# Kernel optimization log

Measured on AMD Instinct MI355X. Metric: run time of the kernel, lower is better.

The kernel has to match this reference:

```python
import jax, jax.numpy as jnp
import numpy as np

B, N, NODE_DIM = 256, 200, 2
H, D, L, FF = 8, 128, 3, 512
KD = D // H  # key/val dim per head = 16
EPS = 1e-5


def _uniform(key, shape, fan):
    s = 1.0 / np.sqrt(fan)
    return jax.random.uniform(key, shape, jnp.float32, -s, s)


def setup_inputs() -> dict:
    key = jax.random.key(0)
    ks = jax.random.split(key, 16)
    return {
        "x": jax.random.normal(ks[0], (B, N, NODE_DIM), jnp.float32),
        "Wemb": _uniform(ks[1], (NODE_DIM, D), NODE_DIM),
        "bemb": _uniform(ks[2], (D,), NODE_DIM),
        "Wq": _uniform(ks[3], (L, H, D, KD), KD),
        "Wk": _uniform(ks[4], (L, H, D, KD), KD),
        "Wv": _uniform(ks[5], (L, H, D, KD), KD),
        "Wo": _uniform(ks[6], (L, H, KD, D), D),
        "bn1_g": jnp.ones((L, D), jnp.float32),
        "bn1_b": jnp.zeros((L, D), jnp.float32),
        "W1": _uniform(ks[7], (L, D, FF), D),
        "b1": _uniform(ks[8], (L, FF), D),
        "W2": _uniform(ks[9], (L, FF, D), FF),
        "b2": _uniform(ks[10], (L, D), FF),
        "bn2_g": jnp.ones((L, D), jnp.float32),
        "bn2_b": jnp.zeros((L, D), jnp.float32),
    }


def _batch_norm(h, g, b):
    # BatchNorm1d in training mode: stats over all (batch*graph) positions per channel
    hf = h.reshape(-1, h.shape[-1])
    m = hf.mean(axis=0)
    v = hf.var(axis=0)  # biased variance, as torch uses for normalization
    return (h - m) * jax.lax.rsqrt(v + EPS) * g + b


def _mha(h, Wq, Wk, Wv, Wo):
    # h: [B,N,D]; Wq/Wk/Wv: [H,D,KD]; Wo: [H,KD,D]
    Q = jnp.einsum('bnd,hdk->hbnk', h, Wq)
    K = jnp.einsum('bnd,hdk->hbnk', h, Wk)
    V = jnp.einsum('bnd,hdk->hbnk', h, Wv)
    scores = jnp.einsum('hbqk,hbnk->hbqn', Q, K) * (1.0 / np.sqrt(KD))
    attn = jax.nn.softmax(scores, axis=-1)
    heads = jnp.einsum('hbqn,hbnk->hbqk', attn, V)
    return jnp.einsum('hbqk,hkd->bqd', heads, Wo)


def reference(x, Wemb, bemb, Wq, Wk, Wv, Wo, bn1_g, bn1_b, W1, b1, W2, b2, bn2_g, bn2_b):
    h = x @ Wemb + bemb  # init_embed: [B,N,D]
    for l in range(L):
        h = h + _mha(h, Wq[l], Wk[l], Wv[l], Wo[l])
        h = _batch_norm(h, bn1_g[l], bn1_b[l])
        ff = jax.nn.relu(h @ W1[l] + b1[l]) @ W2[l] + b2[l]
        h = _batch_norm(h + ff, bn2_g[l], bn2_b[l])
    return (h, h.mean(axis=1))
```

## Files before the change

kernel.cpp:

```cpp
#include <hip/hip_runtime.h>
#include <math.h>

#define B_ 256
#define N_ 200
#define D_ 128
#define H_ 8
#define KD_ 16
#define L_ 3
#define FF_ 512
#define ROWS (B_*N_)
#define BND (ROWS*D_)

typedef float f32x4 __attribute__((ext_vector_type(4)));
typedef _Float16 f16x4 __attribute__((ext_vector_type(4)));
typedef _Float16 f16x8 __attribute__((ext_vector_type(8)));

__device__ __forceinline__ ushort f2h_bits(float f) {
  _Float16 h = (_Float16)f;
  union { _Float16 h; ushort u; } v; v.h = h; return v.u;
}
__device__ __forceinline__ float h2f(ushort u) {
  union { ushort u; _Float16 h; } v; v.u = u; return (float)v.h;
}
__device__ __forceinline__ void bn_reduce(const float* psum, const float* psq,
    const float* gamma, const float* beta, int c, float& sc, float& sh) {
  if (gamma == nullptr) { sc = 1.f; sh = 0.f; return; }
  float s = psum[c], q = psq[c];
  const float invM = 1.f / 51200.f;
  float m = s * invM;
  float v = fmaf(q, invM, -m * m);
  float rr = rsqrtf(v + 1e-5f);
  sc = rr * gamma[c];
  sh = fmaf(-m, sc, beta[c]);
}

__global__ __launch_bounds__(256) void init_kernel(const float* __restrict__ x,
    const float* __restrict__ Wemb, const float* __restrict__ bemb,
    const float* __restrict__ Wo, const float* __restrict__ W2,
    ushort* __restrict__ h, ushort* __restrict__ woT, ushort* __restrict__ w2T,
    float* __restrict__ pa_s, float* __restrict__ pa_q,
    float* __restrict__ pb_s, float* __restrict__ pb_q)
{
  int blk = blockIdx.x, t = threadIdx.x;
  if (blk < 6400) {
    int i4 = blk * 256 + t;
    int r  = i4 >> 5, c4 = i4 & 31;
    float x0 = x[2*r], x1 = x[2*r + 1];
    const float4 w0 = ((const float4*)Wemb)[c4];
    const float4 w1 = ((const float4*)Wemb)[32 + c4];
    const float4 bb = ((const float4*)bemb)[c4];
    ushort o16[4];
    o16[0] = f2h_bits(fmaf(x0, w0.x, fmaf(x1, w1.x, bb.x)));
    o16[1] = f2h_bits(fmaf(x0, w0.y, fmaf(x1, w1.y, bb.y)));
    o16[2] = f2h_bits(fmaf(x0, w0.z, fmaf(x1, w1.z, bb.z)));
    o16[3] = f2h_bits(fmaf(x0, w0.w, fmaf(x1, w1.w, bb.w)));
    uint2 p;
    p.x = (uint)o16[0] | ((uint)o16[1] << 16);
    p.y = (uint)o16[2] | ((uint)o16[3] << 16);
    ((uint2*)h)[i4] = p;
  } else if (blk < 7360) {
    int i = (blk - 6400) * 256 + t;
    if (i < 49152) {
      int l = i / 16384, r = i % 16384;
      int n = r >> 7, k = r & 127;
      int hh = k >> 4, kd = k & 15;
      woT[i] = f2h_bits(Wo[l*16384 + hh*2048 + kd*128 + n]);
    } else {
      int j = i - 49152;
      int l = j / 65536, r = j % 65536;
      int d = r >> 9, f = r & 511;
      w2T[j] = f2h_bits(W2[l*65536 + f*128 + d]);
    }
  } else {
    if (t < 128) { pa_s[t] = 0.f; pa_q[t] = 0.f; pb_s[t] = 0.f; pb_q[t] = 0.f; }
  }
}

__global__ __launch_bounds__(128) void fold_qkv(const float* __restrict__ Wq,
    const float* __restrict__ Wk, const float* __restrict__ Wv,
    const float* __restrict__ pb_s, const float* __restrict__ pb_q,
    const float* __restrict__ gamma, const float* __restrict__ beta,
    ushort* __restrict__ wh, float* __restrict__ bout,
    float* __restrict__ scout, float* __restrict__ shout,
    float* __restrict__ pa_s, float* __restrict__ pa_q)
{
  __shared__ float wsum[2];
  int n = blockIdx.x;
  int k = threadIdx.x;
  float sc, sh;
  bn_reduce(pb_s, pb_q, gamma, beta, k, sc, sh);
  if (n == 0) { scout[k] = sc; shout[k] = sh; }
  if (n == 1) { pa_s[k] = 0.f; pa_q[k] = 0.f; }
  int which = n >> 7, hh = (n >> 4) & 7, kd = n & 15;
  const float* src = (which == 0) ? Wq : (which == 1) ? Wk : Wv;
  float w = src[hh*2048 + k*16 + kd];
  if (which == 0) w *= 0.25f * 1.44269504088896340736f;
  wh[n*128 + k] = f2h_bits(w * sc);
  float p = sh * w;
#pragma unroll
  for (int d = 1; d < 64; d <<= 1) p += __shfl_xor(p, d);
  if ((k & 63) == 0) wsum[k >> 6] = p;
  __syncthreads();
  if (k == 0) bout[n] = wsum[0] + wsum[1];
}

__global__ __launch_bounds__(128) void fold_w1(const float* __restrict__ W1,
    const float* __restrict__ b1,
    const float* __restrict__ pa_s, const float* __restrict__ pa_q,
    const float* __restrict__ gamma, const float* __restrict__ beta,
    ushort* __restrict__ wh, float* __restrict__ bout,
    float* __restrict__ scout, float* __restrict__ shout)
{
  __shared__ float wsum[2];
  int f = blockIdx.x;
  int k = threadIdx.x;
  float sc, sh;
  bn_reduce(pa_s, pa_q, gamma, beta, k, sc, sh);
  if (f == 0) { scout[k] = sc; shout[k] = sh; }
  float w = W1[k*512 + f];
  wh[f*128 + k] = f2h_bits(w * sc);
  float p = sh * w;
#pragma unroll
  for (int d = 1; d < 64; d <<= 1) p += __shfl_xor(p, d);
  if ((k & 63) == 0) wsum[k >> 6] = p;
  __syncthreads();
  if (k == 0) bout[f] = b1[f] + wsum[0] + wsum[1];
}

template<int K, bool BIAS, bool RELU, bool RESIDBN,
         bool OUTQKV, bool OUT16, bool STATS>
__global__ __launch_bounds__(256, 2) void gemm_mfma(
    const ushort* __restrict__ Ah,
    const ushort* __restrict__ Wh,
    const float* __restrict__ bias,
    const ushort* rh,
    const float* __restrict__ rsc, const float* __restrict__ rsh,
    ushort* o0, ushort* o1, ushort* o2,
    float* __restrict__ psum, float* __restrict__ psq, int Ntot)
{
  __shared__ ushort AhS[128*64];
  __shared__ ushort BhS[128*64];
  const int t    = threadIdx.x;
  const int nx   = gridDim.x;
  const int nwg  = nx * gridDim.y;
  const int lin  = blockIdx.y * nx + blockIdx.x;
  const int q8   = nwg >> 3, r8 = nwg & 7;
  const int xcd  = lin & 7, i8 = lin >> 3;
  const int wg   = (xcd < r8 ? xcd*(q8+1) : r8*(q8+1) + (xcd-r8)*q8) + i8;
  const int bm   = (wg / nx) * 128;
  const int bn   = (wg % nx) * 128;
  const int lane = t & 63;
  const int w    = t >> 6, wm = w >> 1, wn = w & 1;
  const int quad = lane >> 4, l15 = lane & 15;

  f32x4 acc[4][4];
#pragma unroll
  for (int i = 0; i < 4; i++)
#pragma unroll
    for (int j = 0; j < 4; j++) acc[i][j] = (f32x4){0.f, 0.f, 0.f, 0.f};

  const ushort* AhB = Ah + (size_t)bm * K;
  const ushort* BhB = Wh + (size_t)bn * K;

  for (int k0 = 0; k0 < K; k0 += 64) {
#pragma unroll
    for (int i = 0; i < 4; i++) {
      int idx = i * 256 + t;
      int row = idx >> 3, c = idx & 7;
      int k8  = c ^ (row & 7);
      size_t off = (size_t)row * K + k0 + k8 * 8;
      ((uint4*)AhS)[idx] = *(const uint4*)(AhB + off);
      ((uint4*)BhS)[idx] = *(const uint4*)(BhB + off);
    }
    __syncthreads();
#pragma unroll
    for (int ks = 0; ks < 2; ks++) {
      f16x8 ah[4], bh[4];
#pragma unroll
      for (int i = 0; i < 4; i++) {
        int row = wm * 64 + i * 16 + l15;
        int k8  = ks * 4 + quad;
        int ci  = k8 ^ (row & 7);
        ah[i] = ((const f16x8*)AhS)[row * 8 + ci];
        int nrow = wn * 64 + i * 16 + l15;
        int cj   = k8 ^ (nrow & 7);
        bh[i] = ((const f16x8*)BhS)[nrow * 8 + cj];
      }
#pragma unroll
      for (int i = 0; i < 4; i++)
#pragma unroll
        for (int j = 0; j < 4; j++)
          acc[i][j] = __builtin_amdgcn_mfma_f32_16x16x32_f16(ah[i], bh[j], acc[i][j], 0, 0, 0);
    }
    __syncthreads();
  }

  float bv[4], scv[4], shv[4];
#pragma unroll
  for (int j = 0; j < 4; j++) {
    int col = bn + wn*64 + j*16 + l15;
    if (BIAS)    bv[j]  = bias[col];
    if (RESIDBN) { scv[j] = rsc[col]; shv[j] = rsh[col]; }
  }
  float sj[4] = {0.f,0.f,0.f,0.f}, qj[4] = {0.f,0.f,0.f,0.f};
#pragma unroll
  for (int i = 0; i < 4; i++) {
#pragma unroll
    for (int r = 0; r < 4; r++) {
      int row = bm + wm*64 + i*16 + quad*4 + r;
#pragma unroll
      for (int j = 0; j < 4; j++) {
        int col = bn + wn*64 + j*16 + l15;
        float v = acc[i][j][r];
        if (BIAS)    v += bv[j];
        if (RELU)    v = fmaxf(v, 0.f);
        if (RESIDBN) {
          float rr = h2f(rh[(size_t)row * Ntot + col]);
          v += fmaf(rr, scv[j], shv[j]);
        }
        if (OUTQKV) {
          if (bn == 0) {
            o0[((size_t)(col >> 4) * ROWS + row) * 16 + (col & 15)] = f2h_bits(v);
          } else if (bn == 128) {
            int c = col - 128;
            o1[((size_t)(c >> 4) * ROWS + row) * 16 + (c & 15)] = f2h_bits(v);
          } else {
            int c = col - 256;
            o2[((size_t)(c >> 4) * ROWS + row) * 16 + (c & 15)] = f2h_bits(v);
          }
        }
        if (OUT16) o0[(size_t)row * Ntot + col] = f2h_bits(v);
        if (STATS) { sj[j] += v; qj[j] = fmaf(v, v, qj[j]); }
      }
    }
  }
  if (STATS) {
#pragma unroll
    for (int j = 0; j < 4; j++) {
      sj[j] += __shfl_xor(sj[j], 16); sj[j] += __shfl_xor(sj[j], 32);
      qj[j] += __shfl_xor(qj[j], 16); qj[j] += __shfl_xor(qj[j], 32);
    }
    float* ssum = (float*)AhS;
    float* ssq  = ssum + 128;
    if (t < 128) { ssum[t] = 0.f; ssq[t] = 0.f; }
    __syncthreads();
    if (quad == 0) {
#pragma unroll
      for (int j = 0; j < 4; j++) {
        int col = wn*64 + j*16 + l15;
        atomicAdd(&ssum[col], sj[j]);
        atomicAdd(&ssq[col],  qj[j]);
      }
    }
    __syncthreads();
    if (t < 128) {
      atomicAdd(&psum[t], ssum[t]);
      atomicAdd(&psq[t],  ssq[t]);
    }
  }
}

__global__ __launch_bounds__(256, 1) void ffn_fused(
    const ushort* __restrict__ h,
    const ushort* __restrict__ w1,
    const float* __restrict__ b1f,
    const ushort* __restrict__ w2t,
    const float* __restrict__ b2,
    const float* __restrict__ rsc, const float* __restrict__ rsh,
    ushort* hout,
    float* __restrict__ psum, float* __restrict__ psq)
{
  __shared__ ushort Ash[2*128*64];
  __shared__ ushort WB [2*128*64];
  __shared__ ushort HB [2*128*72];
  const int t    = threadIdx.x;
  const int bm   = blockIdx.x * 128;
  const int lane = t & 63;
  const int w    = t >> 6, wm = w >> 1, wn = w & 1;
  const int quad = lane >> 4, l15 = lane & 15;

  {
    const ushort* AB = h + (size_t)bm * 128;
    for (int half = 0; half < 2; half++)
#pragma unroll
      for (int i = 0; i < 4; i++) {
        int idx = i * 256 + t;
        int row = idx >> 3, c = idx & 7;
        int k8  = c ^ (row & 7);
        ((uint4*)(Ash + half*8192))[idx] = *(const uint4*)(AB + (size_t)row*128 + half*64 + k8*8);
      }
  }

  f32x4 aco[4][4];
#pragma unroll
  for (int i = 0; i < 4; i++)
#pragma unroll
    for (int j = 0; j < 4; j++) aco[i][j] = (f32x4){0.f, 0.f, 0.f, 0.f};

  __syncthreads();

  for (int ch = 0; ch < 4; ch++) {
    {
      const ushort* W1B = w1 + (size_t)ch * 128 * 128;
      for (int half = 0; half < 2; half++)
#pragma unroll
        for (int i = 0; i < 4; i++) {
          int idx = i * 256 + t;
          int row = idx >> 3, c = idx & 7;
          int k8  = c ^ (row & 7);
          ((uint4*)(WB + half*8192))[idx] = *(const uint4*)(W1B + (size_t)row*128 + half*64 + k8*8);
        }
    }
    __syncthreads();
    f32x4 ach[4][4];
#pragma unroll
    for (int i = 0; i < 4; i++)
#pragma unroll
      for (int j = 0; j < 4; j++) ach[i][j] = (f32x4){0.f, 0.f, 0.f, 0.f};
#pragma unroll
    for (int ks = 0; ks < 4; ks++) {
      int half = ks >> 1, k8 = (ks & 1)*4 + quad;
      f16x8 ah[4], bh[4];
#pragma unroll
      for (int i = 0; i < 4; i++) {
        int row = wm*64 + i*16 + l15;
        int ci  = k8 ^ (row & 7);
        ah[i] = ((const f16x8*)(Ash + half*8192))[row*8 + ci];
        int fr = wn*64 + i*16 + l15;
        int cj  = k8 ^ (fr & 7);
        bh[i] = ((const f16x8*)(WB + half*8192))[fr*8 + cj];
      }
#pragma unroll
      for (int i = 0; i < 4; i++)
#pragma unroll
        for (int j = 0; j < 4; j++)
          ach[i][j] = __builtin_amdgcn_mfma_f32_16x16x32_f16(ah[i], bh[j], ach[i][j], 0, 0, 0);
    }
    __syncthreads();
    {
      float bv1[4];
#pragma unroll
      for (int j = 0; j < 4; j++) bv1[j] = b1f[ch*128 + wn*64 + j*16 + l15];
#pragma unroll
      for (int i = 0; i < 4; i++)
#pragma unroll
        for (int r = 0; r < 4; r++) {
          int row = wm*64 + i*16 + quad*4 + r;
#pragma unroll
          for (int j = 0; j < 4; j++) {
            float hv = fmaxf(ach[i][j][r] + bv1[j], 0.f);
            int k6  = j*16 + l15;
            int ci8 = (k6 >> 3) ^ (row & 7);
            HB[(wn*128 + row)*72 + ci8*8 + (l15 & 7)] = f2h_bits(hv);
          }
        }
    }
    {
      const ushort* W2B = w2t + ch * 128;
      for (int half = 0; half < 2; half++)
#pragma unroll
        for (int i = 0; i < 4; i++) {
          int idx = i * 256 + t;
          int row = idx >> 3, c = idx & 7;
          int k8  = c ^ (row & 7);
          ((uint4*)(WB + half*8192))[idx] = *(const uint4*)(W2B + (size_t)row*512 + half*64 + k8*8);
        }
    }
    __syncthreads();
#pragma unroll
    for (int ks = 0; ks < 4; ks++) {
      int half = ks >> 1, k8 = (ks & 1)*4 + quad;
      f16x8 ah[4], bh[4];
#pragma unroll
      for (int i = 0; i < 4; i++) {
        int row = wm*64 + i*16 + l15;
        int ci  = k8 ^ (row & 7);
        ah[i] = *(const f16x8*)&HB[(half*128 + row)*72 + ci*8];
        int dr = wn*64 + i*16 + l15;
        int cj  = k8 ^ (dr & 7);
        bh[i] = ((const f16x8*)(WB + half*8192))[dr*8 + cj];
      }
#pragma unroll
      for (int i = 0; i < 4; i++)
#pragma unroll
        for (int j = 0; j < 4; j++)
          aco[i][j] = __builtin_amdgcn_mfma_f32_16x16x32_f16(ah[i], bh[j], aco[i][j], 0, 0, 0);
    }
    __syncthreads();
  }

  float bv[4], scv[4], shv[4];
#pragma unroll
  for (int j = 0; j < 4; j++) {
    int col = wn*64 + j*16 + l15;
    bv[j]  = b2[col];
    scv[j] = rsc[col]; shv[j] = rsh[col];
  }
  float sj[4] = {0.f,0.f,0.f,0.f}, qj[4] = {0.f,0.f,0.f,0.f};
#pragma unroll
  for (int i = 0; i < 4; i++) {
#pragma unroll
    for (int r = 0; r < 4; r++) {
      int rloc = wm*64 + i*16 + quad*4 + r;
      int row  = bm + rloc;
#pragma unroll
      for (int j = 0; j < 4; j++) {
        int col = wn*64 + j*16 + l15;
        float v = aco[i][j][r] + bv[j];
        int k6 = col & 63, half = col >> 6;
        int ci = (k6 >> 3) ^ (rloc & 7);
        float rr = h2f(Ash[half*8192 + rloc*64 + ci*8 + (k6 & 7)]);
        v += fmaf(rr, scv[j], shv[j]);
        hout[(size_t)row * 128 + col] = f2h_bits(v);
        sj[j] += v; qj[j] = fmaf(v, v, qj[j]);
      }
    }
  }
#pragma unroll
  for (int j = 0; j < 4; j++) {
    sj[j] += __shfl_xor(sj[j], 16); sj[j] += __shfl_xor(sj[j], 32);
    qj[j] += __shfl_xor(qj[j], 16); qj[j] += __shfl_xor(qj[j], 32);
  }
  __syncthreads();
  float* ssum = (float*)Ash;
  float* ssq  = ssum + 128;
  if (t < 128) { ssum[t] = 0.f; ssq[t] = 0.f; }
  __syncthreads();
  if (quad == 0) {
#pragma unroll
    for (int j = 0; j < 4; j++) {
      int col = wn*64 + j*16 + l15;
      atomicAdd(&ssum[col], sj[j]);
      atomicAdd(&ssq[col],  qj[j]);
    }
  }
  __syncthreads();
  if (t < 128) {
    atomicAdd(&psum[t], ssum[t]);
    atomicAdd(&psq[t],  ssq[t]);
  }
}

__global__ __launch_bounds__(256) void attn_kernel(const ushort* __restrict__ qs,
    const ushort* __restrict__ ks, const ushort* __restrict__ vh,
    ushort* __restrict__ hd, float* __restrict__ pb_s, float* __restrict__ pb_q)
{
  __shared__ __align__(16) _Float16 Ksh[208*24];
  __shared__ __align__(16) _Float16 VTh[16*216];
  const int b  = blockIdx.x >> 3;
  const int hh = blockIdx.x & 7;
  const int t  = threadIdx.x;
  if (blockIdx.x == 0 && t < 128) { pb_s[t] = 0.f; pb_q[t] = 0.f; }
  const size_t rb = (size_t)b * N_;
  const size_t hb = ((size_t)hh * ROWS + rb) * 16;

  for (int i = t; i < 208*2; i += 256) {
    int n = i >> 1, half = i & 1;
    uint4 kv = {0u, 0u, 0u, 0u};
    if (n < N_) kv = *(const uint4*)(ks + hb + n*16 + half*8);
    *(uint4*)&Ksh[n*24 + half*8] = kv;
  }
  for (int i = t; i < 208*2; i += 256) {
    int n = i >> 1, half = i & 1;
    uint4 v0 = {0u, 0u, 0u, 0u};
    if (n < N_) v0 = *(const uint4*)(vh + hb + n*16 + half*8);
    const ushort* e0 = (const ushort*)&v0;
#pragma unroll
    for (int q = 0; q < 8; q++)
      ((ushort*)VTh)[(half*8 + q)*216 + n] = e0[q];
  }
  __syncthreads();

  const int lane = t & 63;
  const int w    = t >> 6;
  const int l15  = lane & 15;
  const int g    = lane >> 4;

  for (int qt = w; qt < 13; qt += 4) {
    int qr  = qt*16 + l15;
    int qrc = qr < N_ ? qr : N_-1;
    f16x4 bq = *(const f16x4*)(qs + hb + (size_t)qrc*16 + g*4);

    f32x4 ct[13];
#pragma unroll
    for (int kt = 0; kt < 13; kt++) {
      f16x4 ak = *(const f16x4*)&Ksh[(kt*16 + l15)*24 + g*4];
      ct[kt] = __builtin_amdgcn_mfma_f32_16x16x16f16(ak, bq, (f32x4){0.f,0.f,0.f,0.f}, 0, 0, 0);
    }
#pragma unroll
    for (int r = 0; r < 4; r++)
      if (g*4 + r >= 8) ct[12][r] = -1e30f;

    float m0 = -1e30f, m1 = -1e30f;
#pragma unroll
    for (int kt = 0; kt < 13; kt++) {
      m0 = fmaxf(m0, fmaxf(ct[kt][0], ct[kt][1]));
      m1 = fmaxf(m1, fmaxf(ct[kt][2], ct[kt][3]));
    }
    float m = fmaxf(m0, m1);
    m = fmaxf(m, __shfl_xor(m, 16));
    m = fmaxf(m, __shfl_xor(m, 32));

    float la0 = 0.f, la1 = 0.f, la2 = 0.f, la3 = 0.f;
#pragma unroll
    for (int kt = 0; kt < 13; kt++) {
      float p0 = __builtin_amdgcn_exp2f(ct[kt][0] - m);
      float p1 = __builtin_amdgcn_exp2f(ct[kt][1] - m);
      float p2 = __builtin_amdgcn_exp2f(ct[kt][2] - m);
      float p3 = __builtin_amdgcn_exp2f(ct[kt][3] - m);
      la0 += p0; la1 += p1; la2 += p2; la3 += p3;
      ct[kt][0] = p0; ct[kt][1] = p1; ct[kt][2] = p2; ct[kt][3] = p3;
    }
    float l = (la0 + la1) + (la2 + la3);
    l += __shfl_xor(l, 16);
    l += __shfl_xor(l, 32);

    f32x4 och = {0.f,0.f,0.f,0.f};
#pragma unroll
    for (int kt = 0; kt < 13; kt++) {
      f16x4 pt = { (_Float16)ct[kt][0], (_Float16)ct[kt][1],
                   (_Float16)ct[kt][2], (_Float16)ct[kt][3] };
      f16x4 avh = *(const f16x4*)&VTh[l15*216 + kt*16 + g*4];
      och = __builtin_amdgcn_mfma_f32_16x16x16f16(avh, pt, och, 0, 0, 0);
    }

    if (qr < N_) {
      float inv = __builtin_amdgcn_rcpf(l);
      ushort o16[4];
#pragma unroll
      for (int r = 0; r < 4; r++) o16[r] = f2h_bits(och[r] * inv);
      uint2 p;
      p.x = (uint)o16[0] | ((uint)o16[1] << 16);
      p.y = (uint)o16[2] | ((uint)o16[3] << 16);
      *(uint2*)(hd + (rb + qr)*128 + hh*16 + g*4) = p;
    }
  }
}

__global__ __launch_bounds__(256) void bn_mean_final(const ushort* __restrict__ h,
    const float* __restrict__ pb_s, const float* __restrict__ pb_q,
    const float* __restrict__ gamma, const float* __restrict__ beta,
    float* __restrict__ outh, float* __restrict__ mout)
{
  __shared__ float part[2][128];
  int b = blockIdx.x;
  int t = threadIdx.x;
  int d = t & 127, half = t >> 7;
  float sc, sh;
  bn_reduce(pb_s, pb_q, gamma, beta, d, sc, sh);
  float s = 0.f;
  for (int n = half*100; n < half*100 + 100; n++) {
    size_t idx = ((size_t)b * N_ + n) * 128 + d;
    float v = fmaf(h2f(h[idx]), sc, sh);
    outh[idx] = v;
    s += v;
  }
  part[half][d] = s;
  __syncthreads();
  if (half == 0) mout[b * 128 + d] = (part[0][d] + part[1][d]) * (1.f / N_);
}

extern "C" void kernel_launch(void* const* d_in, const int* in_sizes, int n_in,
                              void* d_out, int out_size, void* d_ws, size_t ws_size,
                              hipStream_t stream)
{
  const float* x    = (const float*)d_in[0];
  const float* Wemb = (const float*)d_in[1];
  const float* bemb = (const float*)d_in[2];
  const float* Wq   = (const float*)d_in[3];
  const float* Wk   = (const float*)d_in[4];
  const float* Wv   = (const float*)d_in[5];
  const float* Wo   = (const float*)d_in[6];
  const float* bn1g = (const float*)d_in[7];
  const float* bn1b = (const float*)d_in[8];
  const float* W1   = (const float*)d_in[9];
  const float* b1   = (const float*)d_in[10];
  const float* W2   = (const float*)d_in[11];
  const float* b2   = (const float*)d_in[12];
  const float* bn2g = (const float*)d_in[13];
  const float* bn2b = (const float*)d_in[14];
  float* out = (float*)d_out;

  char* wsb = (char*)d_ws;
  ushort* h     = (ushort*)wsb;
  char*   phase = wsb + 13107200;
  ushort* qsb   = (ushort*)phase;
  ushort* ksb   = (ushort*)(phase + 13107200);
  ushort* vhh   = (ushort*)(phase + 26214400);
  ushort* hd    = (ushort*)(phase + 39321600);
  char*   wp    = wsb + 65536000;
  ushort* woT   = (ushort*)wp;
  ushort* w2T   = (ushort*)(wp + 98304);
  ushort* fqkvw = (ushort*)(wp + 491520);
  ushort* fw1w  = (ushort*)(wp + 589824);
  float*  fqkv_b = (float*)(wp + 720896);
  float*  fw1_b  = (float*)(wp + 722432);
  float*  pa_s   = (float*)(wp + 724480);
  float*  pa_q   = (float*)(wp + 724992);
  float*  pb_s   = (float*)(wp + 725504);
  float*  pb_q   = (float*)(wp + 726016);
  float*  sc_a   = (float*)(wp + 726528);
  float*  sh_a   = (float*)(wp + 727040);
  float*  sc_b   = (float*)(wp + 727552);
  float*  sh_b   = (float*)(wp + 728064);

  init_kernel<<<7361, 256, 0, stream>>>(x, Wemb, bemb, Wo, W2, h, woT, w2T,
                                        pa_s, pa_q, pb_s, pb_q);

  for (int l = 0; l < L_; l++) {
    fold_qkv<<<384, 128, 0, stream>>>(Wq + l*16384, Wk + l*16384, Wv + l*16384,
                                      pb_s, pb_q,
                                      l == 0 ? nullptr : bn2g + (l-1)*128,
                                      l == 0 ? nullptr : bn2b + (l-1)*128,
                                      fqkvw, fqkv_b, sc_b, sh_b, pa_s, pa_q);
    gemm_mfma<128, true, false, false, true, false, false>
        <<<dim3(3, 400), 256, 0, stream>>>(
        h, fqkvw, fqkv_b, nullptr, nullptr, nullptr,
        qsb, ksb, vhh, nullptr, nullptr, 384);
    attn_kernel<<<B_ * H_, 256, 0, stream>>>(qsb, ksb, vhh, hd, pb_s, pb_q);
    gemm_mfma<128, false, false, true, false, true, true>
        <<<dim3(1, 400), 256, 0, stream>>>(
        hd, woT + l*16384, nullptr, h, sc_b, sh_b,
        h, nullptr, nullptr, pa_s, pa_q, 128);
    fold_w1<<<512, 128, 0, stream>>>(W1 + l*65536, b1 + l*512,
                                     pa_s, pa_q, bn1g + l*128, bn1b + l*128,
                                     fw1w, fw1_b, sc_a, sh_a);
    ffn_fused<<<400, 256, 0, stream>>>(
        h, fw1w, fw1_b, w2T + l*65536, b2 + l*128, sc_a, sh_a,
        h, pb_s, pb_q);
  }

  bn_mean_final<<<B_, 256, 0, stream>>>(h, pb_s, pb_q,
                                        bn2g + 2*128, bn2b + 2*128, out, out + BND);
}
```

Baseline: 552.1 us.

## Halve FFN row tile to 64 and split columns across four waves

The fused FFN kernel now processes 64 rows per block instead of 128, with each of the four waves owning a 32-column strip rather than a 2x2 wave grid. Grid size doubles to 800 blocks, and launch bounds request 2 blocks per CU thanks to smaller LDS and accumulator footprints. This aims to fill more of the GPU's CUs and raise occupancy for latency hiding. The cost is that W1/W2 weight tiles are reloaded twice as often per row, and each wave reuses fewer B fragments per A load.

```diff
diff --git a/kernel.cpp b/kernel.cpp
--- a/kernel.cpp
+++ b/kernel.cpp
@@ -260,7 +260,7 @@
   }
 }
 
-__global__ __launch_bounds__(256, 1) void ffn_fused(
+__global__ __launch_bounds__(256, 2) void ffn_fused(
     const ushort* __restrict__ h,
     const ushort* __restrict__ w1,
     const float* __restrict__ b1f,
@@ -270,32 +270,32 @@
     ushort* hout,
     float* __restrict__ psum, float* __restrict__ psq)
 {
-  __shared__ ushort Ash[2*128*64];
+  __shared__ ushort Ash[2*64*64];
   __shared__ ushort WB [2*128*64];
-  __shared__ ushort HB [2*128*72];
+  __shared__ ushort HB [2*64*72];
   const int t    = threadIdx.x;
-  const int bm   = blockIdx.x * 128;
+  const int bm   = blockIdx.x * 64;
   const int lane = t & 63;
-  const int w    = t >> 6, wm = w >> 1, wn = w & 1;
+  const int w    = t >> 6;
   const int quad = lane >> 4, l15 = lane & 15;
 
   {
     const ushort* AB = h + (size_t)bm * 128;
     for (int half = 0; half < 2; half++)
 #pragma unroll
-      for (int i = 0; i < 4; i++) {
+      for (int i = 0; i < 2; i++) {
         int idx = i * 256 + t;
         int row = idx >> 3, c = idx & 7;
         int k8  = c ^ (row & 7);
-        ((uint4*)(Ash + half*8192))[idx] = *(const uint4*)(AB + (size_t)row*128 + half*64 + k8*8);
-      }
-  }
-
-  f32x4 aco[4][4];
+        ((uint4*)(Ash + half*4096))[idx] = *(const uint4*)(AB + (size_t)row*128 + half*64 + k8*8);
+      }
+  }
+
+  f32x4 aco[4][2];
 #pragma unroll
   for (int i = 0; i < 4; i++)
 #pragma unroll
-    for (int j = 0; j < 4; j++) aco[i][j] = (f32x4){0.f, 0.f, 0.f, 0.f};
+    for (int j = 0; j < 2; j++) aco[i][j] = (f32x4){0.f, 0.f, 0.f, 0.f};
 
   __syncthreads();
 
@@ -312,46 +312,50 @@
         }
     }
     __syncthreads();
-    f32x4 ach[4][4];
+    f32x4 ach[4][2];
 #pragma unroll
     for (int i = 0; i < 4; i++)
 #pragma unroll
-      for (int j = 0; j < 4; j++) ach[i][j] = (f32x4){0.f, 0.f, 0.f, 0.f};
+      for (int j = 0; j < 2; j++) ach[i][j] = (f32x4){0.f, 0.f, 0.f, 0.f};
 #pragma unroll
     for (int ks = 0; ks < 4; ks++) {
       int half = ks >> 1, k8 = (ks & 1)*4 + quad;
-      f16x8 ah[4], bh[4];
+      f16x8 ah[4], bh[2];
 #pragma unroll
       for (int i = 0; i < 4; i++) {
-        int row = wm*64 + i*16 + l15;
+        int row = i*16 + l15;
         int ci  = k8 ^ (row & 7);
-        ah[i] = ((const f16x8*)(Ash + half*8192))[row*8 + ci];
-        int fr = wn*64 + i*16 + l15;
-        int cj  = k8 ^ (fr & 7);
-        bh[i] = ((const f16x8*)(WB + half*8192))[fr*8 + cj];
+        ah[i] = ((const f16x8*)(Ash + half*4096))[row*8 + ci];
+      }
+#pragma unroll
+      for (int j = 0; j < 2; j++) {
+        int fr = w*32 + j*16 + l15;
+        int cj = k8 ^ (fr & 7);
+        bh[j] = ((const f16x8*)(WB + half*8192))[fr*8 + cj];
       }
 #pragma unroll
       for (int i = 0; i < 4; i++)
 #pragma unroll
-        for (int j = 0; j < 4; j++)
+        for (int j = 0; j < 2; j++)
           ach[i][j] = __builtin_amdgcn_mfma_f32_16x16x32_f16(ah[i], bh[j], ach[i][j], 0, 0, 0);
     }
     __syncthreads();
     {
-      float bv1[4];
-#pragma unroll
-      for (int j = 0; j < 4; j++) bv1[j] = b1f[ch*128 + wn*64 + j*16 + l15];
+      float bv1[2];
+#pragma unroll
+      for (int j = 0; j < 2; j++) bv1[j] = b1f[ch*128 + w*32 + j*16 + l15];
 #pragma unroll
       for (int i = 0; i < 4; i++)
 #pragma unroll
         for (int r = 0; r < 4; r++) {
-          int row = wm*64 + i*16 + quad*4 + r;
-#pragma unroll
-          for (int j = 0; j < 4; j++) {
+          int row = i*16 + quad*4 + r;
+#pragma unroll
+          for (int j = 0; j < 2; j++) {
             float hv = fmaxf(ach[i][j][r] + bv1[j], 0.f);
-            int k6  = j*16 + l15;
+            int f   = w*32 + j*16 + l15;
+            int hf  = f >> 6, k6 = f & 63;
             int ci8 = (k6 >> 3) ^ (row & 7);
-            HB[(wn*128 + row)*72 + ci8*8 + (l15 & 7)] = f2h_bits(hv);
+            HB[hf*4608 + row*72 + ci8*8 + (k6 & 7)] = f2h_bits(hv);
           }
         }
     }
@@ -370,46 +374,49 @@
 #pragma unroll
     for (int ks = 0; ks < 4; ks++) {
       int half = ks >> 1, k8 = (ks & 1)*4 + quad;
-      f16x8 ah[4], bh[4];
+      f16x8 ah[4], bh[2];
 #pragma unroll
       for (int i = 0; i < 4; i++) {
-        int row = wm*64 + i*16 + l15;
+        int row = i*16 + l15;
         int ci  = k8 ^ (row & 7);
-        ah[i] = *(const f16x8*)&HB[(half*128 + row)*72 + ci*8];
-        int dr = wn*64 + i*16 + l15;
-        int cj  = k8 ^ (dr & 7);
-        bh[i] = ((const f16x8*)(WB + half*8192))[dr*8 + cj];
+        ah[i] = *(const f16x8*)&HB[half*4608 + row*72 + ci*8];
+      }
+#pragma unroll
+      for (int j = 0; j < 2; j++) {
+        int dr = w*32 + j*16 + l15;
+        int cj = k8 ^ (dr & 7);
+        bh[j] = ((const f16x8*)(WB + half*8192))[dr*8 + cj];
       }
 #pragma unroll
       for (int i = 0; i < 4; i++)
 #pragma unroll
-        for (int j = 0; j < 4; j++)
+        for (int j = 0; j < 2; j++)
           aco[i][j] = __builtin_amdgcn_mfma_f32_16x16x32_f16(ah[i], bh[j], aco[i][j], 0, 0, 0);
     }
     __syncthreads();
   }
 
-  float bv[4], scv[4], shv[4];
-#pragma unroll
-  for (int j = 0; j < 4; j++) {
-    int col = wn*64 + j*16 + l15;
+  float bv[2], scv[2], shv[2];
+#pragma unroll
+  for (int j = 0; j < 2; j++) {
+    int col = w*32 + j*16 + l15;
     bv[j]  = b2[col];
     scv[j] = rsc[col]; shv[j] = rsh[col];
   }
-  float sj[4] = {0.f,0.f,0.f,0.f}, qj[4] = {0.f,0.f,0.f,0.f};
+  float sj[2] = {0.f,0.f}, qj[2] = {0.f,0.f};
 #pragma unroll
   for (int i = 0; i < 4; i++) {
 #pragma unroll
     for (int r = 0; r < 4; r++) {
-      int rloc = wm*64 + i*16 + quad*4 + r;
+      int rloc = i*16 + quad*4 + r;
       int row  = bm + rloc;
 #pragma unroll
-      for (int j = 0; j < 4; j++) {
-        int col = wn*64 + j*16 + l15;
+      for (int j = 0; j < 2; j++) {
+        int col = w*32 + j*16 + l15;
         float v = aco[i][j][r] + bv[j];
         int k6 = col & 63, half = col >> 6;
         int ci = (k6 >> 3) ^ (rloc & 7);
-        float rr = h2f(Ash[half*8192 + rloc*64 + ci*8 + (k6 & 7)]);
+        float rr = h2f(Ash[half*4096 + rloc*64 + ci*8 + (k6 & 7)]);
         v += fmaf(rr, scv[j], shv[j]);
         hout[(size_t)row * 128 + col] = f2h_bits(v);
         sj[j] += v; qj[j] = fmaf(v, v, qj[j]);
@@ -417,7 +424,7 @@
     }
   }
 #pragma unroll
-  for (int j = 0; j < 4; j++) {
+  for (int j = 0; j < 2; j++) {
     sj[j] += __shfl_xor(sj[j], 16); sj[j] += __shfl_xor(sj[j], 32);
     qj[j] += __shfl_xor(qj[j], 16); qj[j] += __shfl_xor(qj[j], 32);
   }
@@ -428,8 +435,8 @@
   __syncthreads();
   if (quad == 0) {
 #pragma unroll
-    for (int j = 0; j < 4; j++) {
-      int col = wn*64 + j*16 + l15;
+    for (int j = 0; j < 2; j++) {
+      int col = w*32 + j*16 + l15;
       atomicAdd(&ssum[col], sj[j]);
       atomicAdd(&ssq[col],  qj[j]);
     }
@@ -625,7 +632,7 @@
     fold_w1<<<512, 128, 0, stream>>>(W1 + l*65536, b1 + l*512,
                                      pa_s, pa_q, bn1g + l*128, bn1b + l*128,
                                      fw1w, fw1_b, sc_a, sh_a);
-    ffn_fused<<<400, 256, 0, stream>>>(
+    ffn_fused<<<800, 256, 0, stream>>>(
         h, fw1w, fw1_b, w2T + l*65536, b2 + l*128, sc_a, sh_a,
         h, pb_s, pb_q);
   }
```

Result: faster. 500.1 us (median of 3 runs) (-9.4%).
